# Optimization experiments

Hardware: AMD Instinct MI355X
Metric: run time of the kernel (lower is better)

## Reference

```python
import jax, jax.numpy as jnp
import numpy as np

LN_EPS = 1e-5


def setup_inputs() -> dict:
    key = jax.random.key(0)
    ks = jax.random.split(key, 10)
    B, T, D, K = 32, 1024, 512, 3
    enc = jax.random.normal(ks[0], (B, T, D), jnp.float32)
    dur = jax.random.randint(ks[1], (B, T), 0, 7, jnp.int32)
    s = 0.02
    return {
        "encoder_output": enc,
        "duration_target": dur,
        "conv1_w": jax.random.normal(ks[2], (K, D, D), jnp.float32) * s,  # HIO layout
        "conv1_b": jnp.zeros((D,), jnp.float32),
        "ln1_w": jnp.ones((D,), jnp.float32),
        "ln1_b": jnp.zeros((D,), jnp.float32),
        "conv2_w": jax.random.normal(ks[3], (K, D, D), jnp.float32) * s,
        "conv2_b": jnp.zeros((D,), jnp.float32),
        "ln2_w": jnp.ones((D,), jnp.float32),
        "ln2_b": jnp.zeros((D,), jnp.float32),
        "lin_w": jax.random.normal(ks[4], (D, 1), jnp.float32) * s,
        "lin_b": jnp.zeros((1,), jnp.float32),
        "max_len": 4096,
    }


def _conv_relu(x, w, b):
    # x: [B,T,D], w: [K, D_in, D_out] ('HIO'), 'SAME' padding == torch padding=1 for k=3
    y = jax.lax.conv_general_dilated(
        x, w, window_strides=(1,), padding="SAME",
        dimension_numbers=("NHC", "HIO", "NHC"))
    return jax.nn.relu(y + b)


def _layernorm(x, g, b):
    mu = jnp.mean(x, axis=-1, keepdims=True)
    var = jnp.mean(jnp.square(x - mu), axis=-1, keepdims=True)
    return (x - mu) * jax.lax.rsqrt(var + LN_EPS) * g + b


def reference(encoder_output, duration_target, conv1_w, conv1_b, ln1_w, ln1_b,
              conv2_w, conv2_b, ln2_w, ln2_b, lin_w, lin_b, max_len):
    B, T, D = encoder_output.shape
    # duration predictor: conv -> relu -> LN -> conv -> relu -> LN -> linear
    h = _layernorm(_conv_relu(encoder_output, conv1_w, conv1_b), ln1_w, ln1_b)
    h = _layernorm(_conv_relu(h, conv2_w, conv2_b), ln2_w, ln2_b)
    duration_predictor_output = (h @ lin_w + lin_b)[..., 0]  # [B,T]

    # training path: expand by duration_target via fused gather with cumulative offsets
    cum = jnp.cumsum(duration_target, axis=1)          # [B,T]
    pos = jnp.arange(max_len, dtype=jnp.int32)         # [L]
    # src index for output frame j: first t with cum[t] > j
    idx = jax.vmap(lambda c: jnp.searchsorted(c, pos, side="right"))(cum)  # [B,L]
    valid = pos[None, :] < cum[:, -1:]                  # [B,L]
    idx = jnp.minimum(idx, T - 1)
    expanded = jnp.take_along_axis(encoder_output, idx[:, :, None], axis=1)
    expanded = expanded * valid[:, :, None].astype(encoder_output.dtype)
    return expanded, duration_predictor_output
```

## Files before the change

### kernel.cpp

```cpp
#include <hip/hip_runtime.h>
#include <hip/hip_bf16.h>

#define BB 32
#define TT 1024
#define DD 512
#define LL 4096
#define KDIM 1536
#define TP 1026
#define ROWS (BB * TT)
#define NT (KDIM / 32)

typedef __attribute__((ext_vector_type(8))) short short8;
typedef __attribute__((ext_vector_type(8))) unsigned short ushort8;
typedef __attribute__((ext_vector_type(4))) float floatx4;

__device__ __forceinline__ unsigned short f2bf(float f) {
  unsigned int u = __builtin_bit_cast(unsigned int, f);
  u += 0x7FFF + ((u >> 16) & 1);
  return (unsigned short)(u >> 16);
}
__device__ __forceinline__ float bf2f(unsigned short h) {
  return __builtin_bit_cast(float, (unsigned int)h << 16);
}

#define GLOAD_LDS16(g, l)                                          \
  __builtin_amdgcn_global_load_lds(                                \
      (const __attribute__((address_space(1))) void*)(g),          \
      (__attribute__((address_space(3))) void*)(l), 16, 0, 0)

#define PAD_BLKS ((BB * TP) / 4)
__global__ __launch_bounds__(256) void pad_convert_kernel(
    const float* __restrict__ X, unsigned short* __restrict__ Xp,
    unsigned short* __restrict__ Hp) {
  const int lane = threadIdx.x & 63;
  if (blockIdx.x >= PAD_BLKS) {
    const int hid = (blockIdx.x - PAD_BLKS) * 4 + (threadIdx.x >> 6);
    const int b = hid >> 1;
    const long r = (long)b * TP + ((hid & 1) ? (TP - 1) : 0);
    *reinterpret_cast<ushort8*>(Hp + r * DD + lane * 8) = (ushort8)0;
    return;
  }
  const int row = blockIdx.x * 4 + (threadIdx.x >> 6);
  const int b  = row / TP;
  const int pr = row - b * TP;
  ushort8* o = reinterpret_cast<ushort8*>(Xp + (long)row * DD + lane * 8);
  ushort8 v;
  if (pr == 0 || pr == TP - 1) {
    v = (ushort8)0;
  } else {
    const float* p = X + ((long)(b * TT + pr - 1)) * DD + lane * 8;
    float4 a = *reinterpret_cast<const float4*>(p);
    float4 c = *reinterpret_cast<const float4*>(p + 4);
    v[0] = f2bf(a.x); v[1] = f2bf(a.y); v[2] = f2bf(a.z); v[3] = f2bf(a.w);
    v[4] = f2bf(c.x); v[5] = f2bf(c.y); v[6] = f2bf(c.z); v[7] = f2bf(c.w);
  }
  *o = v;
}

__global__ __launch_bounds__(256) void convert_wt_kernel(
    const float* __restrict__ W1, unsigned short* __restrict__ Wt1,
    const float* __restrict__ W2, unsigned short* __restrict__ Wt2) {
  __shared__ float tile[64][65];
  const float* W = (blockIdx.z == 0) ? W1 : W2;
  unsigned short* Wt = (blockIdx.z == 0) ? Wt1 : Wt2;
  const int n0 = blockIdx.x * 64;
  const int k0 = blockIdx.y * 64;
  const int c = threadIdx.x & 63;
  const int r4 = threadIdx.x >> 6;
#pragma unroll
  for (int r = 0; r < 16; ++r) tile[r * 4 + r4][c] = W[(long)(k0 + r * 4 + r4) * DD + n0 + c];
  __syncthreads();
#pragma unroll
  for (int r = 0; r < 16; ++r)
    Wt[(long)(n0 + r * 4 + r4) * KDIM + k0 + c] = f2bf(tile[c][r * 4 + r4]);
}

template <int LAYER>
__global__ __launch_bounds__(512, 2) void fused_conv_ln_kernel(
    const unsigned short* __restrict__ Xp, const unsigned short* __restrict__ Wt,
    const float* __restrict__ bias, const float* __restrict__ g,
    const float* __restrict__ be, const float* __restrict__ lw,
    const float* __restrict__ lb, unsigned short* __restrict__ Hp,
    float* __restrict__ dpo) {
  __shared__ unsigned short As[3][128 * 32];
  __shared__ unsigned short Bs[3][512 * 32];
  __shared__ float sS[4][128];
  __shared__ float sQ[4][128];
  __shared__ float muL[128];
  __shared__ float rsL[128];

  const int tid  = threadIdx.x;
  const int lane = tid & 63;
  const int wid  = tid >> 6;
  const int srow = lane >> 2;
  const int gchunk = (lane & 3) ^ (srow & 3);
  const int frow = lane & 15;
  const int quad = lane >> 4;
  const int rdch = quad ^ (frow & 3);
  const int wm = (wid >> 2) * 64;
  const int wn = (wid & 3) * 128;
  const int wc = wid & 3;

  const int m0 = blockIdx.x * 128;
  const int bA = m0 >> 10;
  const int t0 = m0 & (TT - 1);

  const unsigned short* gA0 =
      Xp + (long)(bA * TP + t0 + wid * 16 + srow) * DD + gchunk * 8;
  const unsigned short* gB0 =
      Wt + (long)(wid * 16 + srow) * KDIM + gchunk * 8;

  floatx4 acc[4][8];
#pragma unroll
  for (int i = 0; i < 4; ++i)
#pragma unroll
    for (int j = 0; j < 8; ++j) acc[i][j] = (floatx4){0.f, 0.f, 0.f, 0.f};

#define STAGE(bi, kk)                                                         \
  do {                                                                        \
    const int tap_ = (kk) >> 9;                                               \
    const int c0_  = (kk) & 511;                                              \
    GLOAD_LDS16(gA0 + (long)tap_ * DD + c0_, &As[bi][(wid * 16) * 32]);       \
    GLOAD_LDS16(gB0 + (kk),                   &Bs[bi][(wid * 16) * 32]);      \
    GLOAD_LDS16(gB0 + (long)128 * KDIM + (kk), &Bs[bi][(128 + wid * 16) * 32]); \
    GLOAD_LDS16(gB0 + (long)256 * KDIM + (kk), &Bs[bi][(256 + wid * 16) * 32]); \
    GLOAD_LDS16(gB0 + (long)384 * KDIM + (kk), &Bs[bi][(384 + wid * 16) * 32]); \
  } while (0)

#define COMPUTE(bi)                                                           \
  do {                                                                        \
    short8 a_[4], b_[8];                                                      \
    _Pragma("unroll")                                                         \
    for (int i = 0; i < 4; ++i)                                               \
      a_[i] = *reinterpret_cast<const short8*>(                               \
          &As[bi][(wm + i * 16 + frow) * 32 + rdch * 8]);                     \
    _Pragma("unroll")                                                         \
    for (int j = 0; j < 8; ++j)                                               \
      b_[j] = *reinterpret_cast<const short8*>(                               \
          &Bs[bi][(wn + j * 16 + frow) * 32 + rdch * 8]);                     \
    _Pragma("unroll")                                                         \
    for (int i = 0; i < 4; ++i)                                               \
      _Pragma("unroll")                                                       \
      for (int j = 0; j < 8; ++j)                                             \
        acc[i][j] = __builtin_amdgcn_mfma_f32_16x16x32_bf16(                  \
            a_[i], b_[j], acc[i][j], 0, 0, 0);                                \
  } while (0)

  STAGE(0, 0);
  STAGE(1, 32);

  int cur = 0;
  int stg = 2;
  for (int t = 0; t < NT - 1; ++t) {
    asm volatile("s_waitcnt vmcnt(5)" ::: "memory");
    __builtin_amdgcn_s_barrier();
    __builtin_amdgcn_sched_barrier(0);
    if (t + 2 < NT) STAGE(stg, (t + 2) * 32);
    COMPUTE(cur);
    cur = (cur == 2) ? 0 : cur + 1;
    stg = (stg == 2) ? 0 : stg + 1;
  }
  asm volatile("s_waitcnt vmcnt(0)" ::: "memory");
  __builtin_amdgcn_s_barrier();
  __builtin_amdgcn_sched_barrier(0);
  COMPUTE(cur);
#undef STAGE
#undef COMPUTE

  float bz[8];
#pragma unroll
  for (int j = 0; j < 8; ++j) bz[j] = bias[wn + j * 16 + frow];
#pragma unroll
  for (int i = 0; i < 4; ++i)
#pragma unroll
    for (int j = 0; j < 8; ++j)
#pragma unroll
      for (int r = 0; r < 4; ++r)
        acc[i][j][r] = fmaxf(acc[i][j][r] + bz[j], 0.f);

  float ps[16], pq[16];
#pragma unroll
  for (int i = 0; i < 4; ++i)
#pragma unroll
    for (int r = 0; r < 4; ++r) {
      float s = 0.f, q = 0.f;
#pragma unroll
      for (int j = 0; j < 8; ++j) {
        const float v = acc[i][j][r];
        s += v; q += v * v;
      }
      ps[i * 4 + r] = s; pq[i * 4 + r] = q;
    }
#pragma unroll
  for (int off = 1; off < 16; off <<= 1)
#pragma unroll
    for (int k = 0; k < 16; ++k) {
      ps[k] += __shfl_xor(ps[k], off);
      pq[k] += __shfl_xor(pq[k], off);
    }
  if (frow == 0) {
#pragma unroll
    for (int i = 0; i < 4; ++i)
#pragma unroll
      for (int r = 0; r < 4; ++r) {
        const int row = wm + i * 16 + quad * 4 + r;
        sS[wc][row] = ps[i * 4 + r];
        sQ[wc][row] = pq[i * 4 + r];
      }
  }
  __syncthreads();
  if (tid < 128) {
    const float s = sS[0][tid] + sS[1][tid] + sS[2][tid] + sS[3][tid];
    const float q = sQ[0][tid] + sQ[1][tid] + sQ[2][tid] + sQ[3][tid];
    const float mu = s * (1.f / DD);
    const float var = q * (1.f / DD) - mu * mu;
    muL[tid] = mu;
    rsL[tid] = rsqrtf(var + 1e-5f);
  }
  __syncthreads();

  float gg[8], bb[8];
#pragma unroll
  for (int j = 0; j < 8; ++j) {
    gg[j] = g[wn + j * 16 + frow];
    bb[j] = be[wn + j * 16 + frow];
  }

  if constexpr (LAYER == 1) {
#pragma unroll
    for (int i = 0; i < 4; ++i)
#pragma unroll
      for (int r = 0; r < 4; ++r) {
        const int row = wm + i * 16 + quad * 4 + r;
        const float mu = muL[row];
        const float rs = rsL[row];
        const long orow = (long)(bA * TP + t0 + row + 1) * DD;
#pragma unroll
        for (int j = 0; j < 8; ++j) {
          const float v = (acc[i][j][r] - mu) * rs * gg[j] + bb[j];
          Hp[orow + wn + j * 16 + frow] = f2bf(v);
        }
      }
  } else {
    float ww[8];
#pragma unroll
    for (int j = 0; j < 8; ++j) ww[j] = lw[wn + j * 16 + frow];
#pragma unroll
    for (int i = 0; i < 4; ++i)
#pragma unroll
      for (int r = 0; r < 4; ++r) {
        const int row = wm + i * 16 + quad * 4 + r;
        const float mu = muL[row];
        const float rs = rsL[row];
        float d = 0.f;
#pragma unroll
        for (int j = 0; j < 8; ++j) {
          const float v = (acc[i][j][r] - mu) * rs * gg[j] + bb[j];
          d += v * ww[j];
        }
#pragma unroll
        for (int off = 1; off < 16; off <<= 1) d += __shfl_xor(d, off);
        if (frow == 0) sS[wc][row] = d;
      }
    __syncthreads();
    if (tid < 128)
      dpo[m0 + tid] =
          sS[0][tid] + sS[1][tid] + sS[2][tid] + sS[3][tid] + lb[0];
  }
}

__global__ __launch_bounds__(1024) void cumsum_kernel(
    const int* __restrict__ dur, int* __restrict__ cum) {
  __shared__ int s[TT];
  const int b = blockIdx.x, t = threadIdx.x;
  s[t] = dur[b * TT + t];
  __syncthreads();
  for (int off = 1; off < TT; off <<= 1) {
    int x = (t >= off) ? s[t - off] : 0;
    __syncthreads();
    s[t] += x;
    __syncthreads();
  }
  cum[b * TT + t] = s[t];
}

__global__ __launch_bounds__(128) void gather_kernel(
    const float* __restrict__ X, const int* __restrict__ cum,
    float* __restrict__ out) {
  const long blk = blockIdx.x;
  const int b = (int)(blk >> 12);
  const int j = (int)(blk & (LL - 1));
  const int* c = cum + b * TT;
  float4* o = reinterpret_cast<float4*>(out + blk * DD) + threadIdx.x;
  const int total = c[TT - 1];
  if (j >= total) {
    *o = make_float4(0.f, 0.f, 0.f, 0.f);
    return;
  }
  int lo = 0, hi = TT - 1;
  while (lo < hi) {
    const int mid = (lo + hi) >> 1;
    if (c[mid] <= j) lo = mid + 1; else hi = mid;
  }
  const float4* src =
      reinterpret_cast<const float4*>(X + ((long)b * TT + lo) * DD) +
      threadIdx.x;
  *o = *src;
}

extern "C" void kernel_launch(void* const* d_in, const int* in_sizes, int n_in,
                              void* d_out, int out_size, void* d_ws,
                              size_t ws_size, hipStream_t stream) {
  const float* enc = (const float*)d_in[0];
  const int* dur   = (const int*)d_in[1];
  const float* w1  = (const float*)d_in[2];
  const float* b1  = (const float*)d_in[3];
  const float* g1  = (const float*)d_in[4];
  const float* be1 = (const float*)d_in[5];
  const float* w2  = (const float*)d_in[6];
  const float* b2  = (const float*)d_in[7];
  const float* g2  = (const float*)d_in[8];
  const float* be2 = (const float*)d_in[9];
  const float* lw  = (const float*)d_in[10];
  const float* lb  = (const float*)d_in[11];

  float* out = (float*)d_out;
  float* expanded = out;
  float* dpo = out + (long)BB * LL * DD;

  unsigned short* enc_pad = (unsigned short*)(expanded);
  unsigned short* h1_pad  = (unsigned short*)(expanded + 9000000);
  unsigned short* wt1     = (unsigned short*)(expanded + 18000000);
  unsigned short* wt2     = (unsigned short*)(expanded + 18400000);
  int* cum = (int*)d_ws;

  pad_convert_kernel<<<PAD_BLKS + 16, 256, 0, stream>>>(enc, enc_pad, h1_pad);
  convert_wt_kernel<<<dim3(DD / 64, KDIM / 64, 2), 256, 0, stream>>>(
      w1, wt1, w2, wt2);

  fused_conv_ln_kernel<1><<<ROWS / 128, 512, 0, stream>>>(
      enc_pad, wt1, b1, g1, be1, nullptr, nullptr, h1_pad, nullptr);
  fused_conv_ln_kernel<2><<<ROWS / 128, 512, 0, stream>>>(
      h1_pad, wt2, b2, g2, be2, lw, lb, nullptr, dpo);

  cumsum_kernel<<<BB, 1024, 0, stream>>>(dur, cum);
  gather_kernel<<<BB * LL, 128, 0, stream>>>(enc, cum, expanded);
}
```

Measured before the change: 529.3 us.

## Merge prep kernels, stage layer-1 output through LDS, batch gather with nontemporal stores

Folds the pad/convert, weight transpose and cumsum launches into one prep kernel, and does the cumsum with a 4-per-thread int4 scan. Layer-1 LayerNorm output is first staged in shared memory (reusing the B tile buffer) so it can be written to global memory as coalesced 16-byte rows instead of scattered 2-byte stores. The gather kernel now handles four frames per 512-thread block and writes with nontemporal stores to cut cache pollution on the large output. The cost is extra barriers in the conv epilogue and one larger kernel with divergent block roles.

```diff
diff --git a/kernel.cpp b/kernel.cpp
--- a/kernel.cpp
+++ b/kernel.cpp
@@ -29,18 +29,67 @@
       (__attribute__((address_space(3))) void*)(l), 16, 0, 0)
 
 #define PAD_BLKS ((BB * TP) / 4)
-__global__ __launch_bounds__(256) void pad_convert_kernel(
+#define W0 (PAD_BLKS + 16)
+#define C0 (W0 + 384)
+#define PREP_BLKS (C0 + 32)
+
+__global__ __launch_bounds__(256) void prep_kernel(
     const float* __restrict__ X, unsigned short* __restrict__ Xp,
-    unsigned short* __restrict__ Hp) {
-  const int lane = threadIdx.x & 63;
+    unsigned short* __restrict__ Hp,
+    const float* __restrict__ W1, unsigned short* __restrict__ Wt1,
+    const float* __restrict__ W2, unsigned short* __restrict__ Wt2,
+    const int* __restrict__ dur, int* __restrict__ cum) {
+  __shared__ float tile[64][65];
+  const int tid = threadIdx.x;
+  const int lane = tid & 63;
+
+  if (blockIdx.x >= C0) {
+    int* ls = reinterpret_cast<int*>(tile);
+    const int b = blockIdx.x - C0;
+    int4 v = reinterpret_cast<const int4*>(dur + b * TT)[tid];
+    const int s0 = v.x, s1 = s0 + v.y, s2 = s1 + v.z, s3 = s2 + v.w;
+    ls[tid] = s3;
+    __syncthreads();
+    for (int off = 1; off < 256; off <<= 1) {
+      int x = (tid >= off) ? ls[tid - off] : 0;
+      __syncthreads();
+      ls[tid] += x;
+      __syncthreads();
+    }
+    const int base = tid ? ls[tid - 1] : 0;
+    int4 o = {base + s0, base + s1, base + s2, base + s3};
+    reinterpret_cast<int4*>(cum + b * TT)[tid] = o;
+    return;
+  }
+  if (blockIdx.x >= W0) {
+    const int w = blockIdx.x - W0;
+    const int z = w / 192;
+    const int rem = w - z * 192;
+    const int bx = rem & 7;
+    const int by = rem >> 3;
+    const float* W = z ? W2 : W1;
+    unsigned short* Wt = z ? Wt2 : Wt1;
+    const int n0 = bx * 64;
+    const int k0 = by * 64;
+    const int c = lane;
+    const int r4 = tid >> 6;
+#pragma unroll
+    for (int r = 0; r < 16; ++r)
+      tile[r * 4 + r4][c] = W[(long)(k0 + r * 4 + r4) * DD + n0 + c];
+    __syncthreads();
+#pragma unroll
+    for (int r = 0; r < 16; ++r)
+      Wt[(long)(n0 + r * 4 + r4) * KDIM + k0 + c] = f2bf(tile[c][r * 4 + r4]);
+    return;
+  }
   if (blockIdx.x >= PAD_BLKS) {
-    const int hid = (blockIdx.x - PAD_BLKS) * 4 + (threadIdx.x >> 6);
+    const int hid = (blockIdx.x - PAD_BLKS) * 4 + (tid >> 6);
     const int b = hid >> 1;
     const long r = (long)b * TP + ((hid & 1) ? (TP - 1) : 0);
     *reinterpret_cast<ushort8*>(Hp + r * DD + lane * 8) = (ushort8)0;
     return;
   }
-  const int row = blockIdx.x * 4 + (threadIdx.x >> 6);
+  const int row = blockIdx.x * 4 + (tid >> 6);
   const int b  = row / TP;
   const int pr = row - b * TP;
   ushort8* o = reinterpret_cast<ushort8*>(Xp + (long)row * DD + lane * 8);
@@ -55,24 +104,6 @@
     v[4] = f2bf(c.x); v[5] = f2bf(c.y); v[6] = f2bf(c.z); v[7] = f2bf(c.w);
   }
   *o = v;
-}
-
-__global__ __launch_bounds__(256) void convert_wt_kernel(
-    const float* __restrict__ W1, unsigned short* __restrict__ Wt1,
-    const float* __restrict__ W2, unsigned short* __restrict__ Wt2) {
-  __shared__ float tile[64][65];
-  const float* W = (blockIdx.z == 0) ? W1 : W2;
-  unsigned short* Wt = (blockIdx.z == 0) ? Wt1 : Wt2;
-  const int n0 = blockIdx.x * 64;
-  const int k0 = blockIdx.y * 64;
-  const int c = threadIdx.x & 63;
-  const int r4 = threadIdx.x >> 6;
-#pragma unroll
-  for (int r = 0; r < 16; ++r) tile[r * 4 + r4][c] = W[(long)(k0 + r * 4 + r4) * DD + n0 + c];
-  __syncthreads();
-#pragma unroll
-  for (int r = 0; r < 16; ++r)
-    Wt[(long)(n0 + r * 4 + r4) * KDIM + k0 + c] = f2bf(tile[c][r * 4 + r4]);
 }
 
 template <int LAYER>
@@ -227,20 +258,37 @@
   }
 
   if constexpr (LAYER == 1) {
-#pragma unroll
-    for (int i = 0; i < 4; ++i)
-#pragma unroll
-      for (int r = 0; r < 4; ++r) {
-        const int row = wm + i * 16 + quad * 4 + r;
-        const float mu = muL[row];
-        const float rs = rsL[row];
-        const long orow = (long)(bA * TP + t0 + row + 1) * DD;
-#pragma unroll
-        for (int j = 0; j < 8; ++j) {
-          const float v = (acc[i][j][r] - mu) * rs * gg[j] + bb[j];
-          Hp[orow + wn + j * 16 + frow] = f2bf(v);
-        }
-      }
+    unsigned short* Ls = &Bs[0][0];
+    const int h = wm >> 6;
+#pragma unroll
+    for (int ph = 0; ph < 2; ++ph) {
+      __syncthreads();
+      if (h == ph) {
+#pragma unroll
+        for (int i = 0; i < 4; ++i)
+#pragma unroll
+          for (int r = 0; r < 4; ++r) {
+            const int row = wm + i * 16 + quad * 4 + r;
+            const float mu = muL[row];
+            const float rs = rsL[row];
+            const int lrow = row - ph * 64;
+#pragma unroll
+            for (int j = 0; j < 8; ++j) {
+              const float v = (acc[i][j][r] - mu) * rs * gg[j] + bb[j];
+              Ls[lrow * 520 + wn + j * 16 + frow] = f2bf(v);
+            }
+          }
+      }
+      __syncthreads();
+      const long gbase = (long)(bA * TP + t0 + ph * 64 + 1) * DD;
+#pragma unroll
+      for (int it = 0; it < 8; ++it) {
+        const int r2 = it * 8 + wid;
+        const int cc = lane * 8;
+        ushort8 val = *reinterpret_cast<const ushort8*>(&Ls[r2 * 520 + cc]);
+        *reinterpret_cast<ushort8*>(&Hp[gbase + (long)r2 * DD + cc]) = val;
+      }
+    }
   } else {
     float ww[8];
 #pragma unroll
@@ -269,32 +317,18 @@
   }
 }
 
-__global__ __launch_bounds__(1024) void cumsum_kernel(
-    const int* __restrict__ dur, int* __restrict__ cum) {
-  __shared__ int s[TT];
-  const int b = blockIdx.x, t = threadIdx.x;
-  s[t] = dur[b * TT + t];
-  __syncthreads();
-  for (int off = 1; off < TT; off <<= 1) {
-    int x = (t >= off) ? s[t - off] : 0;
-    __syncthreads();
-    s[t] += x;
-    __syncthreads();
-  }
-  cum[b * TT + t] = s[t];
-}
-
-__global__ __launch_bounds__(128) void gather_kernel(
+__global__ __launch_bounds__(512) void gather_kernel(
     const float* __restrict__ X, const int* __restrict__ cum,
     float* __restrict__ out) {
-  const long blk = blockIdx.x;
-  const int b = (int)(blk >> 12);
-  const int j = (int)(blk & (LL - 1));
+  const long gf = (long)blockIdx.x * 4 + (threadIdx.x >> 7);
+  const int tl = threadIdx.x & 127;
+  const int b = (int)(gf >> 12);
+  const int j = (int)(gf & (LL - 1));
   const int* c = cum + b * TT;
-  float4* o = reinterpret_cast<float4*>(out + blk * DD) + threadIdx.x;
+  floatx4* o = reinterpret_cast<floatx4*>(out + gf * DD) + tl;
   const int total = c[TT - 1];
   if (j >= total) {
-    *o = make_float4(0.f, 0.f, 0.f, 0.f);
+    __builtin_nontemporal_store((floatx4){0.f, 0.f, 0.f, 0.f}, o);
     return;
   }
   int lo = 0, hi = TT - 1;
@@ -302,10 +336,9 @@
     const int mid = (lo + hi) >> 1;
     if (c[mid] <= j) lo = mid + 1; else hi = mid;
   }
-  const float4* src =
-      reinterpret_cast<const float4*>(X + ((long)b * TT + lo) * DD) +
-      threadIdx.x;
-  *o = *src;
+  const floatx4* src =
+      reinterpret_cast<const floatx4*>(X + ((long)b * TT + lo) * DD) + tl;
+  __builtin_nontemporal_store(*src, o);
 }
 
 extern "C" void kernel_launch(void* const* d_in, const int* in_sizes, int n_in,
@@ -334,15 +367,13 @@
   unsigned short* wt2     = (unsigned short*)(expanded + 18400000);
   int* cum = (int*)d_ws;
 
-  pad_convert_kernel<<<PAD_BLKS + 16, 256, 0, stream>>>(enc, enc_pad, h1_pad);
-  convert_wt_kernel<<<dim3(DD / 64, KDIM / 64, 2), 256, 0, stream>>>(
-      w1, wt1, w2, wt2);
+  prep_kernel<<<PREP_BLKS, 256, 0, stream>>>(enc, enc_pad, h1_pad, w1, wt1,
+                                             w2, wt2, dur, cum);
 
   fused_conv_ln_kernel<1><<<ROWS / 128, 512, 0, stream>>>(
       enc_pad, wt1, b1, g1, be1, nullptr, nullptr, h1_pad, nullptr);
   fused_conv_ln_kernel<2><<<ROWS / 128, 512, 0, stream>>>(
       h1_pad, wt2, b2, g2, be2, lw, lb, nullptr, dpo);
 
-  cumsum_kernel<<<BB, 1024, 0, stream>>>(dur, cum);
-  gather_kernel<<<BB * LL, 128, 0, stream>>>(enc, cum, expanded);
-}
+  gather_kernel<<<BB * LL / 4, 512, 0, stream>>>(enc, cum, expanded);
+}
```

Result: slower. 542.4 us (+2.5%).
